# Optimization experiments

Measured on AMD Instinct MI355X. Metric: run time of the kernel, lower is better.

Reference implementation:

```python
import jax, jax.numpy as jnp
import numpy as np

B, L, D, K = 16, 4096, 256, 64
RHO, LAMBDA_Q, LAMBDA_S = 0.5, 1.0, 1.0


def setup_inputs() -> dict:
    key = jax.random.key(0)
    ks = jax.random.split(key, 16)
    s = 1.0 / np.sqrt(D)
    inp = {
        'q': jax.random.normal(ks[0], (B, D), jnp.float32),
        'r_pos': jax.random.normal(ks[1], (B, D), jnp.float32),
        'r_neg': jax.random.normal(ks[2], (B, D), jnp.float32),
        'h': jax.random.normal(ks[3], (B, L, D), jnp.float32),
        'rp': jax.random.normal(ks[4], (B, L, D), jnp.float32),
        'rn': jax.random.normal(ks[5], (B, L, D), jnp.float32),
        'lengths': jnp.maximum(1, jax.random.randint(ks[6], (B,), 0, L, jnp.int32)),
        'proto_idx': 3,
        'prototypes': jax.random.normal(ks[7], (K, D), jnp.float32),
        'W_hist_w': jax.random.normal(ks[8], (D, 2 * D), jnp.float32) * s,
        'W_hist_b': jnp.zeros((D,), jnp.float32),
        'Wq_w': jax.random.normal(ks[9], (D, D), jnp.float32) * s,
        'Wq_b': jnp.zeros((D,), jnp.float32),
        'Ws_w': jax.random.normal(ks[10], (D, D), jnp.float32) * s,
        'Ws_b': jnp.zeros((D,), jnp.float32),
    }
    return inp


def reference(q, r_pos, r_neg, h, rp, rn, lengths, proto_idx, prototypes,
              W_hist_w, W_hist_b, Wq_w, Wq_b, Ws_w, Ws_b):
    d = q.shape[-1]
    scale = 1.0 / jnp.sqrt(jnp.asarray(d, q.dtype))
    a = prototypes[proto_idx]                                   # [d]
    # gather + tanh-MLP over padded events: inp = [h, rp-rn] -> [B,L,2d]
    inp = jnp.concatenate([h, rp - rn], axis=-1)
    o = jnp.tanh(jnp.einsum('ble,de->bld', inp, W_hist_w) + W_hist_b)  # [B,L,d]
    # attention logits against prototype and query
    logits = (jnp.einsum('bld,d->bl', o, a)
              + RHO * jnp.einsum('bld,bd->bl', o, q)) * scale   # [B,L]
    mask = jnp.arange(o.shape[1])[None, :] < lengths[:, None]   # [B,L]
    logits = jnp.where(mask, logits, -1e30)
    alpha = jax.nn.softmax(logits, axis=1)
    s_q = jnp.einsum('bl,bld->bd', alpha, o)                    # [B,d]
    z = (a[None, :]
         + LAMBDA_Q * (q @ Wq_w.T + Wq_b)
         + LAMBDA_S * (s_q @ Ws_w.T + Ws_b))                    # [B,d]
    delta = jnp.sum(z * (r_pos - r_neg), axis=-1)               # [B]
    # BCE-with-logits against all-ones targets: mean softplus(-delta)
    l_pair = jnp.mean(jax.nn.softplus(-delta))
    return l_pair
```

## Files before the change

kernel.cpp:

```cpp
#include <hip/hip_runtime.h>

#define B_      16
#define L_      4096
#define D_      256
#define K2_     512
#define TILE_M  64
#define BK      64
#define KITERS  8
#define PSTRIDE 264

typedef float f32x4 __attribute__((ext_vector_type(4)));
typedef short bf16x8 __attribute__((ext_vector_type(8)));

__device__ __forceinline__ unsigned short f2bf(float x) {
    unsigned int u = __float_as_uint(x);
    u += 0x7FFF + ((u >> 16) & 1);
    return (unsigned short)(u >> 16);
}

__device__ __forceinline__ void gload_lds16(const void* g, void* l) {
    __builtin_amdgcn_global_load_lds(
        (const __attribute__((address_space(1))) unsigned int*)g,
        (__attribute__((address_space(3))) unsigned int*)l, 16, 0, 0);
}

__device__ __forceinline__ float fast_tanh(float x) {
    float e = __expf(2.0f * x);
    return 1.0f - __fdividef(2.0f, e + 1.0f);
}

__global__ __launch_bounds__(256) void prep_kernel(
    const float* __restrict__ Wh, const float* __restrict__ protos,
    const float* __restrict__ q, const int* __restrict__ pidx,
    unsigned short* __restrict__ wsW, float* __restrict__ aeff)
{
    const int blk = blockIdx.x, tid = threadIdx.x;
    if (blk < 256) {
        int d  = blk;
        int e  = tid * 2;
        int t  = e >> 6;
        int kk = e & 63;
        float2 w = *reinterpret_cast<const float2*>(Wh + d * K2_ + e);
        unsigned int v = (unsigned int)f2bf(w.x) | ((unsigned int)f2bf(w.y) << 16);
        int dst = t * 32768 + ((d * 128 + kk * 2) ^ ((d & 7) << 4));
        *reinterpret_cast<unsigned int*>(reinterpret_cast<char*>(wsW) + dst) = v;
    } else {
        int b = blk - 256;
        int d = tid;
        int pi = pidx[0];
        aeff[b * D_ + d] = (protos[pi * D_ + d] + 0.5f * q[b * D_ + d]) * 0.0625f;
    }
}

__global__ __launch_bounds__(256, 2) void main_kernel(
    const float* __restrict__ h, const float* __restrict__ rp, const float* __restrict__ rn,
    const int* __restrict__ lengths, const unsigned short* __restrict__ wsW,
    const float* __restrict__ aeff, const float* __restrict__ bhist,
    float* __restrict__ partials)
{
    const int bid = blockIdx.x;
    const int b   = bid >> 6;
    const int t   = bid & 63;
    const int len = lengths[b];
    const int l0  = t * TILE_M;
    if (l0 >= len) return;

    __shared__ __align__(16) char SM[81920];

    const int tid  = threadIdx.x;
    const int lane = tid & 63;
    const int wv   = tid >> 6;
    const int r16  = lane & 15;
    const int kg   = lane >> 4;

    const int ar  = tid >> 2;
    const int akk = (tid & 3) * 16;
    const int s0  = (ar * 128 + akk * 2) ^ ((ar & 7) << 4);
    const int s1  = (ar * 128 + akk * 2 + 16) ^ ((ar & 7) << 4);

    const f32x4 zero4 = {0.f, 0.f, 0.f, 0.f};
    f32x4 acc[4][4];
#pragma unroll
    for (int m = 0; m < 4; ++m)
#pragma unroll
        for (int n = 0; n < 4; ++n) acc[m][n] = zero4;

    f32x4 ra[4], rb[4];

    auto stageB = [&](int buf, int tk) {
        const char* bsrc = reinterpret_cast<const char*>(wsW) + tk * 32768;
        char* dst = SM + 16384 + buf * 32768;
#pragma unroll
        for (int i = 0; i < 8; ++i) {
            int off = i * 4096 + wv * 1024;
            gload_lds16(bsrc + off + lane * 16, dst + off);
        }
    };
    auto loadA = [&](int tk) {
        if (tk < 4) {
            const float* src = h + ((size_t)(b * L_ + l0 + ar)) * D_ + tk * 64 + akk;
#pragma unroll
            for (int i = 0; i < 4; ++i) ra[i] = reinterpret_cast<const f32x4*>(src)[i];
        } else {
            size_t o0 = ((size_t)(b * L_ + l0 + ar)) * D_ + (tk - 4) * 64 + akk;
#pragma unroll
            for (int i = 0; i < 4; ++i) ra[i] = reinterpret_cast<const f32x4*>(rp + o0)[i];
#pragma unroll
            for (int i = 0; i < 4; ++i) rb[i] = reinterpret_cast<const f32x4*>(rn + o0)[i];
        }
    };
    auto writeA = [&](int buf, int tk) {
        float vals[16];
        if (tk < 4) {
#pragma unroll
            for (int i = 0; i < 4; ++i)
#pragma unroll
                for (int j = 0; j < 4; ++j) vals[i * 4 + j] = ra[i][j];
        } else {
#pragma unroll
            for (int i = 0; i < 4; ++i)
#pragma unroll
                for (int j = 0; j < 4; ++j) vals[i * 4 + j] = ra[i][j] - rb[i][j];
        }
        unsigned int pk[8];
#pragma unroll
        for (int i = 0; i < 8; ++i)
            pk[i] = (unsigned int)f2bf(vals[2 * i]) | ((unsigned int)f2bf(vals[2 * i + 1]) << 16);
        char* Ab = SM + buf * 8192;
        *reinterpret_cast<uint4*>(Ab + s0) = make_uint4(pk[0], pk[1], pk[2], pk[3]);
        *reinterpret_cast<uint4*>(Ab + s1) = make_uint4(pk[4], pk[5], pk[6], pk[7]);
    };
    auto computeT = [&](int buf) {
        const char* Ab = SM + buf * 8192;
        const char* Bb = SM + 16384 + buf * 32768;
#pragma unroll
        for (int ks = 0; ks < 2; ++ks) {
            const int kk = ks * 32 + kg * 8;
            bf16x8 af[4], bf[4];
#pragma unroll
            for (int m = 0; m < 4; ++m) {
                int row = m * 16 + r16;
                int off = (row * 128 + kk * 2) ^ ((row & 7) << 4);
                af[m] = *reinterpret_cast<const bf16x8*>(Ab + off);
            }
#pragma unroll
            for (int n = 0; n < 4; ++n) {
                int d = wv * 64 + n * 16 + r16;
                int off = (d * 128 + kk * 2) ^ ((d & 7) << 4);
                bf[n] = *reinterpret_cast<const bf16x8*>(Bb + off);
            }
#pragma unroll
            for (int m = 0; m < 4; ++m)
#pragma unroll
                for (int n = 0; n < 4; ++n)
                    acc[m][n] = __builtin_amdgcn_mfma_f32_16x16x32_bf16(af[m], bf[n], acc[m][n], 0, 0, 0);
        }
    };

    loadA(0);
    stageB(0, 0);
    writeA(0, 0);
    __syncthreads();

    int buf = 0;
    for (int tk = 0; tk < KITERS; ++tk) {
        const bool pf = (tk + 1) < KITERS;
        if (pf) { stageB(buf ^ 1, tk + 1); loadA(tk + 1); }
        computeT(buf);
        if (pf) writeA(buf ^ 1, tk + 1);
        __syncthreads();
        buf ^= 1;
    }

    float* red  = reinterpret_cast<float*>(SM);
    float* pbuf = reinterpret_cast<float*>(SM + 1024);

    float av[4], bh[4];
#pragma unroll
    for (int n = 0; n < 4; ++n) {
        int col = wv * 64 + n * 16 + r16;
        av[n] = aeff[b * D_ + col];
        bh[n] = bhist[col];
    }
    float part[4][4];
#pragma unroll
    for (int m = 0; m < 4; ++m)
#pragma unroll
        for (int rg = 0; rg < 4; ++rg) part[m][rg] = 0.f;
#pragma unroll
    for (int m = 0; m < 4; ++m)
#pragma unroll
        for (int n = 0; n < 4; ++n)
#pragma unroll
            for (int rg = 0; rg < 4; ++rg) {
                float o = fast_tanh(acc[m][n][rg] + bh[n]);
                acc[m][n][rg] = o;
                part[m][rg] += o * av[n];
            }
#pragma unroll
    for (int off = 1; off < 16; off <<= 1)
#pragma unroll
        for (int m = 0; m < 4; ++m)
#pragma unroll
            for (int rg = 0; rg < 4; ++rg)
                part[m][rg] += __shfl_xor(part[m][rg], off, 64);
    if (r16 == 0) {
#pragma unroll
        for (int m = 0; m < 4; ++m)
#pragma unroll
            for (int rg = 0; rg < 4; ++rg)
                red[wv * 64 + m * 16 + kg * 4 + rg] = part[m][rg];
    }
    __syncthreads();

    float* pout = partials + (size_t)(b * 64 + t) * PSTRIDE;
    if (tid < 64) {
        int row = tid;
        float lg = red[row] + red[64 + row] + red[128 + row] + red[192 + row];
        bool valid = (l0 + row) < len;
        float mv = valid ? lg : -3.0e38f;
#pragma unroll
        for (int off = 1; off < 64; off <<= 1)
            mv = fmaxf(mv, __shfl_xor(mv, off, 64));
        float p = valid ? __expf(lg - mv) : 0.f;
        float sa = p;
#pragma unroll
        for (int off = 1; off < 64; off <<= 1)
            sa += __shfl_xor(sa, off, 64);
        pbuf[row] = p;
        if (tid == 0) { pout[0] = mv; pout[1] = sa; }
    }
    __syncthreads();

    float so[4] = {0.f, 0.f, 0.f, 0.f};
#pragma unroll
    for (int m = 0; m < 4; ++m)
#pragma unroll
        for (int rg = 0; rg < 4; ++rg) {
            float p = pbuf[m * 16 + kg * 4 + rg];
#pragma unroll
            for (int n = 0; n < 4; ++n)
                so[n] += p * acc[m][n][rg];
        }
#pragma unroll
    for (int n = 0; n < 4; ++n) {
        so[n] += __shfl_xor(so[n], 16, 64);
        so[n] += __shfl_xor(so[n], 32, 64);
    }
    if (lane < 16) {
#pragma unroll
        for (int n = 0; n < 4; ++n)
            pout[2 + wv * 64 + n * 16 + lane] = so[n];
    }
}

__global__ __launch_bounds__(256) void reduce_kernel(
    const float* __restrict__ partials, const int* __restrict__ lengths,
    const float* __restrict__ protos, const int* __restrict__ pidx,
    const float* __restrict__ q,
    const float* __restrict__ Wq_w, const float* __restrict__ Wq_b,
    const float* __restrict__ Ws_w, const float* __restrict__ Ws_b,
    const float* __restrict__ rpos, const float* __restrict__ rneg,
    float* __restrict__ out)
{
    const int b   = blockIdx.x;
    const int tid = threadIdx.x;
    const int lane = tid & 63;
    const int wv   = tid >> 6;
    const int len = lengths[b];
    const int nT  = (len + TILE_M - 1) / TILE_M;

    __shared__ __align__(16) float mArr[64];
    __shared__ __align__(16) float sAArr[64];
    __shared__ __align__(16) float sq[D_];
    __shared__ __align__(16) float qlds[D_];
    __shared__ __align__(16) float zbuf[D_];
    __shared__ float wsum[4];

    const float* pbase = partials + (size_t)b * 64 * PSTRIDE;
    if (tid < nT) {
        mArr[tid]  = pbase[(size_t)tid * PSTRIDE];
        sAArr[tid] = pbase[(size_t)tid * PSTRIDE + 1];
    }
    qlds[tid] = q[b * D_ + tid];
    __syncthreads();

    float M = -3.0e38f;
    for (int t = 0; t < nT; ++t) M = fmaxf(M, mArr[t]);
    float den = 0.f, num = 0.f;
    for (int t = 0; t < nT; ++t) {
        float f = __expf(mArr[t] - M);
        den += f * sAArr[t];
        num += f * pbase[(size_t)t * PSTRIDE + 2 + tid];
    }
    sq[tid] = num / den;
    __syncthreads();

    const int c = lane & 3;
    const float4* q4 = reinterpret_cast<const float4*>(qlds) + c * 16;
    const float4* s4 = reinterpret_cast<const float4*>(sq) + c * 16;
#pragma unroll
    for (int p = 0; p < 4; ++p) {
        int drow = p * 64 + wv * 16 + (lane >> 2);
        const float4* wq4 = reinterpret_cast<const float4*>(Wq_w + (size_t)drow * D_) + c * 16;
        const float4* ws4 = reinterpret_cast<const float4*>(Ws_w + (size_t)drow * D_) + c * 16;
        float a = 0.f;
#pragma unroll 4
        for (int i = 0; i < 16; ++i) {
            float4 wq = wq4[i], ws = ws4[i], qv = q4[i], sv = s4[i];
            a += wq.x * qv.x + wq.y * qv.y + wq.z * qv.z + wq.w * qv.w;
            a += ws.x * sv.x + ws.y * sv.y + ws.z * sv.z + ws.w * sv.w;
        }
        a += __shfl_xor(a, 1, 64);
        a += __shfl_xor(a, 2, 64);
        if (c == 0) zbuf[drow] = a;
    }
    __syncthreads();

    const int pi = pidx[0];
    float zd = protos[pi * D_ + tid] + Wq_b[tid] + Ws_b[tid] + zbuf[tid];
    float v = zd * (rpos[b * D_ + tid] - rneg[b * D_ + tid]);
#pragma unroll
    for (int off = 1; off < 64; off <<= 1) v += __shfl_xor(v, off, 64);
    if (lane == 0) wsum[wv] = v;
    __syncthreads();
    if (tid == 0) {
        float delta = wsum[0] + wsum[1] + wsum[2] + wsum[3];
        float x = -delta;
        float sp = fmaxf(x, 0.f) + log1pf(__expf(-fabsf(x)));
        atomicAdd(out, sp * (1.0f / (float)B_));
    }
}

extern "C" void kernel_launch(void* const* d_in, const int* in_sizes, int n_in,
                              void* d_out, int out_size, void* d_ws, size_t ws_size,
                              hipStream_t stream) {
    const float* q       = (const float*)d_in[0];
    const float* r_pos   = (const float*)d_in[1];
    const float* r_neg   = (const float*)d_in[2];
    const float* h       = (const float*)d_in[3];
    const float* rp      = (const float*)d_in[4];
    const float* rn      = (const float*)d_in[5];
    const int*   lengths = (const int*)d_in[6];
    const int*   pidx    = (const int*)d_in[7];
    const float* protos  = (const float*)d_in[8];
    const float* Wh_w    = (const float*)d_in[9];
    const float* Wh_b    = (const float*)d_in[10];
    const float* Wq_w    = (const float*)d_in[11];
    const float* Wq_b    = (const float*)d_in[12];
    const float* Ws_w    = (const float*)d_in[13];
    const float* Ws_b    = (const float*)d_in[14];
    float* out = (float*)d_out;

    char* ws = (char*)d_ws;
    unsigned short* wsW = (unsigned short*)ws;
    float* aeff     = (float*)(ws + 262144);
    float* partials = (float*)(ws + 278528);

    hipMemsetAsync(out, 0, sizeof(float), stream);
    prep_kernel<<<dim3(272), dim3(256), 0, stream>>>(Wh_w, protos, q, pidx, wsW, aeff);
    main_kernel<<<dim3(B_ * 64), dim3(256), 0, stream>>>(h, rp, rn, lengths, wsW, aeff, Wh_b, partials);
    reduce_kernel<<<dim3(B_), dim3(256), 0, stream>>>(partials, lengths, protos, pidx, q,
                                                      Wq_w, Wq_b, Ws_w, Ws_b, r_pos, r_neg, out);
}
```

Baseline: 253.3 us.

## Compact valid tiles, load A directly into MFMA registers, split reduce into kernels

A prep block now builds a compacted list of valid (batch, tile) pairs, so main-kernel blocks map only to tiles that hold real rows instead of launching and early-exiting on padded ones. The A operand is loaded from global straight into MFMA fragment registers and converted to bf16 in registers, which removes the A LDS staging buffer and its writes. The warp layout changes to 2x2 (row group by column half) with 8 N-tiles per wave, and a sched_barrier is added before compute. The tail reduce is split into sq, z and final kernels, with z spreading the projection over 256 blocks; this adds launches and reuses the weight workspace region for scratch.

```diff
diff --git a/kernel.cpp b/kernel.cpp
--- a/kernel.cpp
+++ b/kernel.cpp
@@ -17,13 +17,20 @@
     u += 0x7FFF + ((u >> 16) & 1);
     return (unsigned short)(u >> 16);
 }
-
+__device__ __forceinline__ unsigned int pk2(float a, float b) {
+    return (unsigned int)f2bf(a) | ((unsigned int)f2bf(b) << 16);
+}
+__device__ __forceinline__ bf16x8 pack8(f32x4 a, f32x4 b) {
+    union { bf16x8 v; unsigned int u[4]; } r;
+    r.u[0] = pk2(a[0], a[1]); r.u[1] = pk2(a[2], a[3]);
+    r.u[2] = pk2(b[0], b[1]); r.u[3] = pk2(b[2], b[3]);
+    return r.v;
+}
 __device__ __forceinline__ void gload_lds16(const void* g, void* l) {
     __builtin_amdgcn_global_load_lds(
         (const __attribute__((address_space(1))) unsigned int*)g,
         (__attribute__((address_space(3))) unsigned int*)l, 16, 0, 0);
 }
-
 __device__ __forceinline__ float fast_tanh(float x) {
     float e = __expf(2.0f * x);
     return 1.0f - __fdividef(2.0f, e + 1.0f);
@@ -32,7 +39,9 @@
 __global__ __launch_bounds__(256) void prep_kernel(
     const float* __restrict__ Wh, const float* __restrict__ protos,
     const float* __restrict__ q, const int* __restrict__ pidx,
-    unsigned short* __restrict__ wsW, float* __restrict__ aeff)
+    const int* __restrict__ lengths,
+    unsigned short* __restrict__ wsW, float* __restrict__ aeff,
+    int* __restrict__ tiles, int* __restrict__ tileCnt)
 {
     const int blk = blockIdx.x, tid = threadIdx.x;
     if (blk < 256) {
@@ -41,14 +50,28 @@
         int t  = e >> 6;
         int kk = e & 63;
         float2 w = *reinterpret_cast<const float2*>(Wh + d * K2_ + e);
-        unsigned int v = (unsigned int)f2bf(w.x) | ((unsigned int)f2bf(w.y) << 16);
+        unsigned int v = pk2(w.x, w.y);
         int dst = t * 32768 + ((d * 128 + kk * 2) ^ ((d & 7) << 4));
         *reinterpret_cast<unsigned int*>(reinterpret_cast<char*>(wsW) + dst) = v;
-    } else {
+    } else if (blk < 272) {
         int b = blk - 256;
         int d = tid;
         int pi = pidx[0];
         aeff[b * D_ + d] = (protos[pi * D_ + d] + 0.5f * q[b * D_ + d]) * 0.0625f;
+    } else {
+        int nT = 0;
+        if (tid < B_) nT = min(64, (lengths[tid] + TILE_M - 1) / TILE_M);
+        int pre = 0, tot = 0;
+#pragma unroll
+        for (int j = 0; j < B_; ++j) {
+            int v = __shfl(nT, j, 64);
+            tot += v;
+            if (j < tid) pre += v;
+        }
+        if (tid < B_) {
+            for (int t = 0; t < nT; ++t) tiles[pre + t] = (tid << 16) | t;
+        }
+        if (tid == 0) tileCnt[0] = tot;
     }
 }
 
@@ -56,40 +79,45 @@
     const float* __restrict__ h, const float* __restrict__ rp, const float* __restrict__ rn,
     const int* __restrict__ lengths, const unsigned short* __restrict__ wsW,
     const float* __restrict__ aeff, const float* __restrict__ bhist,
-    float* __restrict__ partials)
+    float* __restrict__ partials, const int* __restrict__ tiles,
+    const int* __restrict__ tileCnt)
 {
     const int bid = blockIdx.x;
-    const int b   = bid >> 6;
-    const int t   = bid & 63;
+    if (bid >= tileCnt[0]) return;
+    const int ent = tiles[bid];
+    const int b   = ent >> 16;
+    const int t   = ent & 0xFFFF;
     const int len = lengths[b];
     const int l0  = t * TILE_M;
-    if (l0 >= len) return;
-
-    __shared__ __align__(16) char SM[81920];
+
+    __shared__ __align__(16) char Bsm[65536];
+    __shared__ float red[128];
+    __shared__ float pbuf[64];
+    __shared__ float solds[4 * 128];
 
     const int tid  = threadIdx.x;
     const int lane = tid & 63;
     const int wv   = tid >> 6;
+    const int rg   = wv >> 1;
+    const int ch   = wv & 1;
     const int r16  = lane & 15;
     const int kg   = lane >> 4;
 
-    const int ar  = tid >> 2;
-    const int akk = (tid & 3) * 16;
-    const int s0  = (ar * 128 + akk * 2) ^ ((ar & 7) << 4);
-    const int s1  = (ar * 128 + akk * 2 + 16) ^ ((ar & 7) << 4);
+    const size_t rowA0 = ((size_t)b * L_ + l0 + rg * 32 + r16) * D_ + kg * 8;
 
     const f32x4 zero4 = {0.f, 0.f, 0.f, 0.f};
-    f32x4 acc[4][4];
-#pragma unroll
-    for (int m = 0; m < 4; ++m)
-#pragma unroll
-        for (int n = 0; n < 4; ++n) acc[m][n] = zero4;
-
-    f32x4 ra[4], rb[4];
+    f32x4 acc[2][8];
+#pragma unroll
+    for (int m = 0; m < 2; ++m)
+#pragma unroll
+        for (int n = 0; n < 8; ++n) acc[m][n] = zero4;
+
+    f32x4 pA[2][2][2], pB[2][2][2];
+    bf16x8 frag[2][2];
 
     auto stageB = [&](int buf, int tk) {
         const char* bsrc = reinterpret_cast<const char*>(wsW) + tk * 32768;
-        char* dst = SM + 16384 + buf * 32768;
+        char* dst = Bsm + buf * 32768;
 #pragma unroll
         for (int i = 0; i < 8; ++i) {
             int off = i * 4096 + wv * 1024;
@@ -98,125 +126,115 @@
     };
     auto loadA = [&](int tk) {
         if (tk < 4) {
-            const float* src = h + ((size_t)(b * L_ + l0 + ar)) * D_ + tk * 64 + akk;
-#pragma unroll
-            for (int i = 0; i < 4; ++i) ra[i] = reinterpret_cast<const f32x4*>(src)[i];
+            const float* p0 = h + rowA0 + tk * 64;
+#pragma unroll
+            for (int m = 0; m < 2; ++m) {
+                const float* p = p0 + m * 16 * D_;
+#pragma unroll
+                for (int ks = 0; ks < 2; ++ks) {
+                    pA[m][ks][0] = *reinterpret_cast<const f32x4*>(p + ks * 32);
+                    pA[m][ks][1] = *reinterpret_cast<const f32x4*>(p + ks * 32 + 4);
+                }
+            }
         } else {
-            size_t o0 = ((size_t)(b * L_ + l0 + ar)) * D_ + (tk - 4) * 64 + akk;
-#pragma unroll
-            for (int i = 0; i < 4; ++i) ra[i] = reinterpret_cast<const f32x4*>(rp + o0)[i];
-#pragma unroll
-            for (int i = 0; i < 4; ++i) rb[i] = reinterpret_cast<const f32x4*>(rn + o0)[i];
+            size_t o0 = rowA0 + (tk - 4) * 64;
+#pragma unroll
+            for (int m = 0; m < 2; ++m) {
+                size_t o = o0 + (size_t)m * 16 * D_;
+#pragma unroll
+                for (int ks = 0; ks < 2; ++ks) {
+                    pA[m][ks][0] = *reinterpret_cast<const f32x4*>(rp + o + ks * 32);
+                    pA[m][ks][1] = *reinterpret_cast<const f32x4*>(rp + o + ks * 32 + 4);
+                    pB[m][ks][0] = *reinterpret_cast<const f32x4*>(rn + o + ks * 32);
+                    pB[m][ks][1] = *reinterpret_cast<const f32x4*>(rn + o + ks * 32 + 4);
+                }
+            }
         }
     };
-    auto writeA = [&](int buf, int tk) {
-        float vals[16];
-        if (tk < 4) {
-#pragma unroll
-            for (int i = 0; i < 4; ++i)
-#pragma unroll
-                for (int j = 0; j < 4; ++j) vals[i * 4 + j] = ra[i][j];
-        } else {
-#pragma unroll
-            for (int i = 0; i < 4; ++i)
-#pragma unroll
-                for (int j = 0; j < 4; ++j) vals[i * 4 + j] = ra[i][j] - rb[i][j];
-        }
-        unsigned int pk[8];
-#pragma unroll
-        for (int i = 0; i < 8; ++i)
-            pk[i] = (unsigned int)f2bf(vals[2 * i]) | ((unsigned int)f2bf(vals[2 * i + 1]) << 16);
-        char* Ab = SM + buf * 8192;
-        *reinterpret_cast<uint4*>(Ab + s0) = make_uint4(pk[0], pk[1], pk[2], pk[3]);
-        *reinterpret_cast<uint4*>(Ab + s1) = make_uint4(pk[4], pk[5], pk[6], pk[7]);
+    auto cvtA = [&](int tk) {
+#pragma unroll
+        for (int m = 0; m < 2; ++m)
+#pragma unroll
+            for (int ks = 0; ks < 2; ++ks) {
+                f32x4 v0, v1;
+                if (tk < 4) { v0 = pA[m][ks][0]; v1 = pA[m][ks][1]; }
+                else        { v0 = pA[m][ks][0] - pB[m][ks][0]; v1 = pA[m][ks][1] - pB[m][ks][1]; }
+                frag[m][ks] = pack8(v0, v1);
+            }
     };
     auto computeT = [&](int buf) {
-        const char* Ab = SM + buf * 8192;
-        const char* Bb = SM + 16384 + buf * 32768;
+        const char* Bb = Bsm + buf * 32768;
 #pragma unroll
         for (int ks = 0; ks < 2; ++ks) {
-            const int kk = ks * 32 + kg * 8;
-            bf16x8 af[4], bf[4];
-#pragma unroll
-            for (int m = 0; m < 4; ++m) {
-                int row = m * 16 + r16;
-                int off = (row * 128 + kk * 2) ^ ((row & 7) << 4);
-                af[m] = *reinterpret_cast<const bf16x8*>(Ab + off);
+#pragma unroll
+            for (int nt = 0; nt < 8; ++nt) {
+                int d   = ch * 128 + nt * 16 + r16;
+                int off = (d * 128 + (ks * 32 + kg * 8) * 2) ^ ((d & 7) << 4);
+                bf16x8 bfr = *reinterpret_cast<const bf16x8*>(Bb + off);
+                acc[0][nt] = __builtin_amdgcn_mfma_f32_16x16x32_bf16(frag[0][ks], bfr, acc[0][nt], 0, 0, 0);
+                acc[1][nt] = __builtin_amdgcn_mfma_f32_16x16x32_bf16(frag[1][ks], bfr, acc[1][nt], 0, 0, 0);
             }
-#pragma unroll
-            for (int n = 0; n < 4; ++n) {
-                int d = wv * 64 + n * 16 + r16;
-                int off = (d * 128 + kk * 2) ^ ((d & 7) << 4);
-                bf[n] = *reinterpret_cast<const bf16x8*>(Bb + off);
-            }
-#pragma unroll
-            for (int m = 0; m < 4; ++m)
-#pragma unroll
-                for (int n = 0; n < 4; ++n)
-                    acc[m][n] = __builtin_amdgcn_mfma_f32_16x16x32_bf16(af[m], bf[n], acc[m][n], 0, 0, 0);
         }
     };
 
     loadA(0);
     stageB(0, 0);
-    writeA(0, 0);
+    cvtA(0);
     __syncthreads();
 
     int buf = 0;
     for (int tk = 0; tk < KITERS; ++tk) {
         const bool pf = (tk + 1) < KITERS;
-        if (pf) { stageB(buf ^ 1, tk + 1); loadA(tk + 1); }
+        if (pf) { loadA(tk + 1); stageB(buf ^ 1, tk + 1); }
+        __builtin_amdgcn_sched_barrier(0);
         computeT(buf);
-        if (pf) writeA(buf ^ 1, tk + 1);
+        if (pf) cvtA(tk + 1);
         __syncthreads();
         buf ^= 1;
     }
 
-    float* red  = reinterpret_cast<float*>(SM);
-    float* pbuf = reinterpret_cast<float*>(SM + 1024);
-
-    float av[4], bh[4];
-#pragma unroll
-    for (int n = 0; n < 4; ++n) {
-        int col = wv * 64 + n * 16 + r16;
-        av[n] = aeff[b * D_ + col];
-        bh[n] = bhist[col];
-    }
-    float part[4][4];
-#pragma unroll
-    for (int m = 0; m < 4; ++m)
-#pragma unroll
-        for (int rg = 0; rg < 4; ++rg) part[m][rg] = 0.f;
-#pragma unroll
-    for (int m = 0; m < 4; ++m)
-#pragma unroll
-        for (int n = 0; n < 4; ++n)
-#pragma unroll
-            for (int rg = 0; rg < 4; ++rg) {
-                float o = fast_tanh(acc[m][n][rg] + bh[n]);
-                acc[m][n][rg] = o;
-                part[m][rg] += o * av[n];
+    float av[8], bh[8];
+#pragma unroll
+    for (int nt = 0; nt < 8; ++nt) {
+        int col = ch * 128 + nt * 16 + r16;
+        av[nt] = aeff[b * D_ + col];
+        bh[nt] = bhist[col];
+    }
+    float part[2][4];
+#pragma unroll
+    for (int m = 0; m < 2; ++m)
+#pragma unroll
+        for (int rgi = 0; rgi < 4; ++rgi) part[m][rgi] = 0.f;
+#pragma unroll
+    for (int m = 0; m < 2; ++m)
+#pragma unroll
+        for (int nt = 0; nt < 8; ++nt)
+#pragma unroll
+            for (int rgi = 0; rgi < 4; ++rgi) {
+                float o = fast_tanh(acc[m][nt][rgi] + bh[nt]);
+                acc[m][nt][rgi] = o;
+                part[m][rgi] += o * av[nt];
             }
 #pragma unroll
     for (int off = 1; off < 16; off <<= 1)
 #pragma unroll
-        for (int m = 0; m < 4; ++m)
-#pragma unroll
-            for (int rg = 0; rg < 4; ++rg)
-                part[m][rg] += __shfl_xor(part[m][rg], off, 64);
+        for (int m = 0; m < 2; ++m)
+#pragma unroll
+            for (int rgi = 0; rgi < 4; ++rgi)
+                part[m][rgi] += __shfl_xor(part[m][rgi], off, 64);
     if (r16 == 0) {
 #pragma unroll
-        for (int m = 0; m < 4; ++m)
-#pragma unroll
-            for (int rg = 0; rg < 4; ++rg)
-                red[wv * 64 + m * 16 + kg * 4 + rg] = part[m][rg];
+        for (int m = 0; m < 2; ++m)
+#pragma unroll
+            for (int rgi = 0; rgi < 4; ++rgi)
+                red[ch * 64 + rg * 32 + m * 16 + kg * 4 + rgi] = part[m][rgi];
     }
     __syncthreads();
 
     float* pout = partials + (size_t)(b * 64 + t) * PSTRIDE;
     if (tid < 64) {
         int row = tid;
-        float lg = red[row] + red[64 + row] + red[128 + row] + red[192 + row];
+        float lg = red[row] + red[64 + row];
         bool valid = (l0 + row) < len;
         float mv = valid ? lg : -3.0e38f;
 #pragma unroll
@@ -232,34 +250,98 @@
     }
     __syncthreads();
 
-    float so[4] = {0.f, 0.f, 0.f, 0.f};
-#pragma unroll
-    for (int m = 0; m < 4; ++m)
-#pragma unroll
-        for (int rg = 0; rg < 4; ++rg) {
-            float p = pbuf[m * 16 + kg * 4 + rg];
-#pragma unroll
-            for (int n = 0; n < 4; ++n)
-                so[n] += p * acc[m][n][rg];
-        }
-#pragma unroll
-    for (int n = 0; n < 4; ++n) {
-        so[n] += __shfl_xor(so[n], 16, 64);
-        so[n] += __shfl_xor(so[n], 32, 64);
+    float so[8];
+#pragma unroll
+    for (int nt = 0; nt < 8; ++nt) so[nt] = 0.f;
+#pragma unroll
+    for (int m = 0; m < 2; ++m)
+#pragma unroll
+        for (int rgi = 0; rgi < 4; ++rgi) {
+            float p = pbuf[rg * 32 + m * 16 + kg * 4 + rgi];
+#pragma unroll
+            for (int nt = 0; nt < 8; ++nt)
+                so[nt] += p * acc[m][nt][rgi];
+        }
+#pragma unroll
+    for (int nt = 0; nt < 8; ++nt) {
+        so[nt] += __shfl_xor(so[nt], 16, 64);
+        so[nt] += __shfl_xor(so[nt], 32, 64);
     }
     if (lane < 16) {
 #pragma unroll
-        for (int n = 0; n < 4; ++n)
-            pout[2 + wv * 64 + n * 16 + lane] = so[n];
-    }
-}
-
-__global__ __launch_bounds__(256) void reduce_kernel(
+        for (int nt = 0; nt < 8; ++nt)
+            solds[wv * 128 + nt * 16 + lane] = so[nt];
+    }
+    __syncthreads();
+    {
+        int col = tid;
+        int c2  = col >> 7, cl = col & 127;
+        pout[2 + col] = solds[c2 * 128 + cl] + solds[(2 + c2) * 128 + cl];
+    }
+}
+
+__global__ __launch_bounds__(256) void sq_kernel(
     const float* __restrict__ partials, const int* __restrict__ lengths,
+    float* __restrict__ sqout)
+{
+    const int b   = blockIdx.x;
+    const int tid = threadIdx.x;
+    const int len = lengths[b];
+    const int nT  = min(64, (len + TILE_M - 1) / TILE_M);
+
+    __shared__ float mArr[64];
+    __shared__ float sAArr[64];
+
+    const float* pbase = partials + (size_t)b * 64 * PSTRIDE;
+    if (tid < nT) {
+        mArr[tid]  = pbase[(size_t)tid * PSTRIDE];
+        sAArr[tid] = pbase[(size_t)tid * PSTRIDE + 1];
+    }
+    __syncthreads();
+
+    float M = -3.0e38f;
+    for (int t = 0; t < nT; ++t) M = fmaxf(M, mArr[t]);
+    float den = 0.f, num = 0.f;
+    for (int t = 0; t < nT; ++t) {
+        float f = __expf(mArr[t] - M);
+        den += f * sAArr[t];
+        num += f * pbase[(size_t)t * PSTRIDE + 2 + tid];
+    }
+    sqout[b * D_ + tid] = num / den;
+}
+
+__global__ __launch_bounds__(256) void z_kernel(
+    const float* __restrict__ q, const float* __restrict__ sq,
     const float* __restrict__ protos, const int* __restrict__ pidx,
-    const float* __restrict__ q,
     const float* __restrict__ Wq_w, const float* __restrict__ Wq_b,
     const float* __restrict__ Ws_w, const float* __restrict__ Ws_b,
+    float* __restrict__ zout)
+{
+    const int r   = blockIdx.x;
+    const int tid = threadIdx.x;
+    const int bb  = tid >> 4;
+    const int c   = tid & 15;
+    const float4* wq = reinterpret_cast<const float4*>(Wq_w + (size_t)r * D_) + c * 4;
+    const float4* ws = reinterpret_cast<const float4*>(Ws_w + (size_t)r * D_) + c * 4;
+    const float4* qv = reinterpret_cast<const float4*>(q  + bb * D_) + c * 4;
+    const float4* sv = reinterpret_cast<const float4*>(sq + bb * D_) + c * 4;
+    float a = 0.f;
+#pragma unroll
+    for (int i = 0; i < 4; ++i) {
+        float4 w1 = wq[i], w2 = ws[i], v1 = qv[i], v2 = sv[i];
+        a += w1.x * v1.x + w1.y * v1.y + w1.z * v1.z + w1.w * v1.w;
+        a += w2.x * v2.x + w2.y * v2.y + w2.z * v2.z + w2.w * v2.w;
+    }
+#pragma unroll
+    for (int off = 1; off < 16; off <<= 1) a += __shfl_xor(a, off, 64);
+    if (c == 0) {
+        int pi = pidx[0];
+        zout[bb * D_ + r] = protos[pi * D_ + r] + Wq_b[r] + Ws_b[r] + a;
+    }
+}
+
+__global__ __launch_bounds__(256) void final_kernel(
+    const float* __restrict__ zbuf,
     const float* __restrict__ rpos, const float* __restrict__ rneg,
     float* __restrict__ out)
 {
@@ -267,59 +349,8 @@
     const int tid = threadIdx.x;
     const int lane = tid & 63;
     const int wv   = tid >> 6;
-    const int len = lengths[b];
-    const int nT  = (len + TILE_M - 1) / TILE_M;
-
-    __shared__ __align__(16) float mArr[64];
-    __shared__ __align__(16) float sAArr[64];
-    __shared__ __align__(16) float sq[D_];
-    __shared__ __align__(16) float qlds[D_];
-    __shared__ __align__(16) float zbuf[D_];
     __shared__ float wsum[4];
-
-    const float* pbase = partials + (size_t)b * 64 * PSTRIDE;
-    if (tid < nT) {
-        mArr[tid]  = pbase[(size_t)tid * PSTRIDE];
-        sAArr[tid] = pbase[(size_t)tid * PSTRIDE + 1];
-    }
-    qlds[tid] = q[b * D_ + tid];
-    __syncthreads();
-
-    float M = -3.0e38f;
-    for (int t = 0; t < nT; ++t) M = fmaxf(M, mArr[t]);
-    float den = 0.f, num = 0.f;
-    for (int t = 0; t < nT; ++t) {
-        float f = __expf(mArr[t] - M);
-        den += f * sAArr[t];
-        num += f * pbase[(size_t)t * PSTRIDE + 2 + tid];
-    }
-    sq[tid] = num / den;
-    __syncthreads();
-
-    const int c = lane & 3;
-    const float4* q4 = reinterpret_cast<const float4*>(qlds) + c * 16;
-    const float4* s4 = reinterpret_cast<const float4*>(sq) + c * 16;
-#pragma unroll
-    for (int p = 0; p < 4; ++p) {
-        int drow = p * 64 + wv * 16 + (lane >> 2);
-        const float4* wq4 = reinterpret_cast<const float4*>(Wq_w + (size_t)drow * D_) + c * 16;
-        const float4* ws4 = reinterpret_cast<const float4*>(Ws_w + (size_t)drow * D_) + c * 16;
-        float a = 0.f;
-#pragma unroll 4
-        for (int i = 0; i < 16; ++i) {
-            float4 wq = wq4[i], ws = ws4[i], qv = q4[i], sv = s4[i];
-            a += wq.x * qv.x + wq.y * qv.y + wq.z * qv.z + wq.w * qv.w;
-            a += ws.x * sv.x + ws.y * sv.y + ws.z * sv.z + ws.w * sv.w;
-        }
-        a += __shfl_xor(a, 1, 64);
-        a += __shfl_xor(a, 2, 64);
-        if (c == 0) zbuf[drow] = a;
-    }
-    __syncthreads();
-
-    const int pi = pidx[0];
-    float zd = protos[pi * D_ + tid] + Wq_b[tid] + Ws_b[tid] + zbuf[tid];
-    float v = zd * (rpos[b * D_ + tid] - rneg[b * D_ + tid]);
+    float v = zbuf[b * D_ + tid] * (rpos[b * D_ + tid] - rneg[b * D_ + tid]);
 #pragma unroll
     for (int off = 1; off < 64; off <<= 1) v += __shfl_xor(v, off, 64);
     if (lane == 0) wsum[wv] = v;
@@ -356,10 +387,18 @@
     unsigned short* wsW = (unsigned short*)ws;
     float* aeff     = (float*)(ws + 262144);
     float* partials = (float*)(ws + 278528);
+    int*   tiles    = (int*)(ws + 1359872);
+    int*   tileCnt  = (int*)(ws + 1363968);
+    float* sqws     = (float*)ws;
+    float* zbuf     = (float*)(ws + 16384);
 
     hipMemsetAsync(out, 0, sizeof(float), stream);
-    prep_kernel<<<dim3(272), dim3(256), 0, stream>>>(Wh_w, protos, q, pidx, wsW, aeff);
-    main_kernel<<<dim3(B_ * 64), dim3(256), 0, stream>>>(h, rp, rn, lengths, wsW, aeff, Wh_b, partials);
-    reduce_kernel<<<dim3(B_), dim3(256), 0, stream>>>(partials, lengths, protos, pidx, q,
-                                                      Wq_w, Wq_b, Ws_w, Ws_b, r_pos, r_neg, out);
-}
+    prep_kernel<<<dim3(273), dim3(256), 0, stream>>>(Wh_w, protos, q, pidx, lengths,
+                                                     wsW, aeff, tiles, tileCnt);
+    main_kernel<<<dim3(B_ * 64), dim3(256), 0, stream>>>(h, rp, rn, lengths, wsW, aeff, Wh_b,
+                                                         partials, tiles, tileCnt);
+    sq_kernel<<<dim3(B_), dim3(256), 0, stream>>>(partials, lengths, sqws);
+    z_kernel<<<dim3(256), dim3(256), 0, stream>>>(q, sqws, protos, pidx,
+                                                  Wq_w, Wq_b, Ws_w, Ws_b, zbuf);
+    final_kernel<<<dim3(B_), dim3(256), 0, stream>>>(zbuf, r_pos, r_neg, out);
+}
```

Measured after the change: 245.0 us. 3.3% less time.
